# Kernel optimization log

Measured on AMD Instinct MI355X. Metric: run time of the kernel, lower is better.

The kernel has to match this reference:

```python
import jax, jax.numpy as jnp
import numpy as np

N = 50000   # nodes
E = 640000  # edges
IN, H, OUT = 128, 128, 64
BN_EPS = 1e-5


def setup_inputs() -> dict:
    key = jax.random.key(0)
    ks = jax.random.split(key, 16)
    inp = {}
    inp["x"] = jax.random.normal(ks[0], (N, IN), jnp.float32)
    inp["edge_index"] = jax.random.randint(ks[1], (2, E), 0, N, dtype=jnp.int32)
    # BatchNorm affine params (nontrivial so grads are informative)
    inp["bn_in_gamma"] = 1.0 + 0.1 * jax.random.normal(ks[2], (IN,), jnp.float32)
    inp["bn_in_beta"] = 0.1 * jax.random.normal(ks[3], (IN,), jnp.float32)
    inp["bn1_gamma"] = 1.0 + 0.1 * jax.random.normal(ks[4], (H,), jnp.float32)
    inp["bn1_beta"] = 0.1 * jax.random.normal(ks[5], (H,), jnp.float32)
    inp["bn2_gamma"] = 1.0 + 0.1 * jax.random.normal(ks[6], (OUT,), jnp.float32)
    inp["bn2_beta"] = 0.1 * jax.random.normal(ks[7], (OUT,), jnp.float32)
    # Linear / GCNConv weights (fan-in scaled)
    inp["proj_W"] = jax.random.normal(ks[8], (IN, H), jnp.float32) / np.sqrt(IN)
    inp["proj_b"] = jnp.zeros((H,), jnp.float32)
    inp["conv1_W"] = jax.random.normal(ks[9], (H, H), jnp.float32) / np.sqrt(H)
    inp["conv1_b"] = jnp.zeros((H,), jnp.float32)
    inp["conv2_W"] = jax.random.normal(ks[10], (H, OUT), jnp.float32) / np.sqrt(H)
    inp["conv2_b"] = jnp.zeros((OUT,), jnp.float32)
    return inp


def batchnorm(x, gamma, beta):
    # training-mode BN: batch statistics (biased variance), per-feature affine
    m = jnp.mean(x, axis=0)
    v = jnp.mean(jnp.square(x - m), axis=0)
    return (x - m) * jax.lax.rsqrt(v + BN_EPS) * gamma + beta


def gcn_conv(x, src, dst, W, b):
    # PyG GCNConv: y = D^{-1/2} (A + I) D^{-1/2} (x W) + b
    xw = x @ W                                    # [N, F_out]
    loops = jnp.arange(N, dtype=src.dtype)
    s = jnp.concatenate([src, loops])             # [E + N]
    d = jnp.concatenate([dst, loops])
    deg = jax.ops.segment_sum(jnp.ones_like(d, jnp.float32), d, num_segments=N)
    dinv = jnp.where(deg > 0, jax.lax.rsqrt(deg), 0.0)
    norm = dinv[s] * dinv[d]                      # [E + N]
    msgs = xw[s] * norm[:, None]                  # gather + per-edge scale
    out = jax.ops.segment_sum(msgs, d, num_segments=N)  # scatter-add
    return out + b


def reference(x, edge_index, bn_in_gamma, bn_in_beta, bn1_gamma, bn1_beta,
              bn2_gamma, bn2_beta, proj_W, proj_b, conv1_W, conv1_b,
              conv2_W, conv2_b):
    src, dst = edge_index[0], edge_index[1]
    h = batchnorm(x, bn_in_gamma, bn_in_beta)
    h = jax.nn.relu(h @ proj_W + proj_b)
    h = jax.nn.relu(batchnorm(gcn_conv(h, src, dst, conv1_W, conv1_b),
                              bn1_gamma, bn1_beta))
    # dropout: identity in eval mode
    out = batchnorm(gcn_conv(h, src, dst, conv2_W, conv2_b),
                    bn2_gamma, bn2_beta)
    return out
```

## Files before the change

kernel.cpp:

```cpp
#include <hip/hip_runtime.h>

#define NN 50000
#define NE 640000
#define BNEPS 1e-5f
#define NBANK 16
#define CAP 64

#define OFF_DINV 0
#define OFF_CURSOR 51200
#define OFF_ESRC 102400
#define OFF_WT0 1702400
#define OFF_WT1 1710592
#define OFF_WT2 1718784
#define OFF_STATS 1726976
#define OFF_B0 1737216
#define OFF_B1 8137216

typedef __attribute__((ext_vector_type(8))) __bf16 bf16x8;
typedef __attribute__((ext_vector_type(4))) float f32x4;

__device__ __forceinline__ float uplo(unsigned int u) {
  unsigned int v = u << 16;
  return __builtin_bit_cast(float, v);
}
__device__ __forceinline__ float uphi(unsigned int u) {
  unsigned int v = u & 0xffff0000u;
  return __builtin_bit_cast(float, v);
}
__device__ __forceinline__ unsigned int f2bf(float f) {
  unsigned int u = __builtin_bit_cast(unsigned int, f);
  return (u + 0x7fffu + ((u >> 16) & 1u)) >> 16;
}

__global__ __launch_bounds__(256) void prep_k(
    const float* __restrict__ W0, const float* __restrict__ W1,
    const float* __restrict__ W2, unsigned short* __restrict__ T0,
    unsigned short* __restrict__ T1, unsigned short* __restrict__ T2,
    int* __restrict__ cursor, float* __restrict__ stats) {
  const int bid = blockIdx.x;
  const int tid = threadIdx.x;
  if (bid < 160) {
    int f = bid * 256 + tid;
    if (f < 16384) {
      int k = f >> 7, n = f & 127;
      T0[n * 128 + k] = (unsigned short)f2bf(W0[f]);
    } else if (f < 32768) {
      int g = f - 16384;
      int k = g >> 7, n = g & 127;
      T1[n * 128 + k] = (unsigned short)f2bf(W1[g]);
    } else if (f < 40960) {
      int g = f - 32768;
      int k = g >> 6, n = g & 63;
      T2[n * 128 + k] = (unsigned short)f2bf(W2[g]);
    }
  } else if (bid < 356) {
    int i = (bid - 160) * 256 + tid;
    if (i < NN) cursor[i] = i * CAP;
  } else {
    int j = (bid - 356) * 256 + tid;
    stats[j] = 0.0f;
  }
}

template <int NC, int MODE>
__device__ __forceinline__ void bn_stats_body(
    int sbid, int nsb, int tid, const float* __restrict__ A,
    const float* __restrict__ dinv, const float* __restrict__ cb,
    float* __restrict__ sums, float* __restrict__ sqs,
    float (*rs)[NC], float (*rq)[NC]) {
  constexpr int CG = NC / 4;
  constexpr int RG = 256 / CG;
  const int tc = tid % CG;
  const int tr = tid / CG;
  float cb0 = 0, cb1 = 0, cb2 = 0, cb3 = 0;
  if (MODE == 1) {
    cb0 = cb[tc * 4];
    cb1 = cb[tc * 4 + 1];
    cb2 = cb[tc * 4 + 2];
    cb3 = cb[tc * 4 + 3];
  }
  float s0 = 0, s1 = 0, s2 = 0, s3 = 0, q0 = 0, q1 = 0, q2 = 0, q3 = 0;
  const int stride = nsb * RG;
  for (int r = sbid * RG + tr; r < NN; r += stride) {
    float4 v = *(const float4*)&A[(size_t)r * NC + tc * 4];
    if (MODE == 1) {
      float di = dinv[r];
      v.x = fmaf(v.x, di, cb0);
      v.y = fmaf(v.y, di, cb1);
      v.z = fmaf(v.z, di, cb2);
      v.w = fmaf(v.w, di, cb3);
    }
    s0 += v.x; s1 += v.y; s2 += v.z; s3 += v.w;
    q0 += v.x * v.x; q1 += v.y * v.y; q2 += v.z * v.z; q3 += v.w * v.w;
  }
  rs[tr][tc * 4] = s0; rs[tr][tc * 4 + 1] = s1;
  rs[tr][tc * 4 + 2] = s2; rs[tr][tc * 4 + 3] = s3;
  rq[tr][tc * 4] = q0; rq[tr][tc * 4 + 1] = q1;
  rq[tr][tc * 4 + 2] = q2; rq[tr][tc * 4 + 3] = q3;
  __syncthreads();
  if (tr == 0) {
    const int bank = (sbid & (NBANK - 1)) * NC;
    for (int j = 0; j < 4; ++j) {
      int c = tc * 4 + j;
      float ts = 0, tq = 0;
      for (int g = 0; g < RG; ++g) { ts += rs[g][c]; tq += rq[g][c]; }
      atomicAdd(&sums[bank + c], ts);
      atomicAdd(&sqs[bank + c], tq);
    }
  }
}

template <int NC, int MODE>
__global__ __launch_bounds__(256) void bn_stats_k(const float* __restrict__ A,
                                                  const float* __restrict__ dinv,
                                                  const float* __restrict__ cb,
                                                  float* __restrict__ sums,
                                                  float* __restrict__ sqs) {
  __shared__ float rs[256 / (NC / 4)][NC];
  __shared__ float rq[256 / (NC / 4)][NC];
  bn_stats_body<NC, MODE>(blockIdx.x, gridDim.x, threadIdx.x, A, dinv, cb,
                          sums, sqs, rs, rq);
}

__global__ __launch_bounds__(256) void bn_stats_bf_k(
    const unsigned short* __restrict__ Z, float* __restrict__ sums,
    float* __restrict__ sqs) {
  const int tc = threadIdx.x % 16;
  const int tr = threadIdx.x / 16;
  const int c = tc * 8;
  float s[8], q[8];
#pragma unroll
  for (int j = 0; j < 8; ++j) { s[j] = 0.f; q[j] = 0.f; }
  const int stride = gridDim.x * 16;
  for (int r = blockIdx.x * 16 + tr; r < NN; r += stride) {
    const uint4 p = *(const uint4*)&Z[(size_t)r * 128 + c];
    float e[8] = {uplo(p.x), uphi(p.x), uplo(p.y), uphi(p.y),
                  uplo(p.z), uphi(p.z), uplo(p.w), uphi(p.w)};
#pragma unroll
    for (int j = 0; j < 8; ++j) { s[j] += e[j]; q[j] += e[j] * e[j]; }
  }
  __shared__ float rs[16][128];
  __shared__ float rq[16][128];
#pragma unroll
  for (int j = 0; j < 8; ++j) { rs[tr][c + j] = s[j]; rq[tr][c + j] = q[j]; }
  __syncthreads();
  if (tr == 0) {
    const int bank = (blockIdx.x & (NBANK - 1)) * 128;
#pragma unroll
    for (int j = 0; j < 8; ++j) {
      float ts = 0.f, tq = 0.f;
      for (int g = 0; g < 16; ++g) { ts += rs[g][c + j]; tq += rq[g][c + j]; }
      atomicAdd(&sums[bank + c + j], ts);
      atomicAdd(&sqs[bank + c + j], tq);
    }
  }
}

template <int NC, int PRE, int EPI>
__device__ __forceinline__ void gemm_body(
    int bid, int tid, char* __restrict__ smem, float* __restrict__ af_s,
    float* __restrict__ bf_s, const void* __restrict__ Ain,
    const unsigned short* __restrict__ Wt, const float* __restrict__ bias,
    const float* __restrict__ sums, const float* __restrict__ sqs,
    const float* __restrict__ gamma, const float* __restrict__ beta,
    unsigned short* __restrict__ O1) {
  constexpr int TM = 64;
  constexpr int NTILES = NC / 16;
  constexpr int CSTR = NC + 4;
  const int row0 = bid * TM;

  if constexpr (PRE != 1) {
    if (tid < 128) {
      float s = 0.f, q = 0.f;
#pragma unroll
      for (int b = 0; b < NBANK; ++b) {
        s += sums[b * 128 + tid];
        q += sqs[b * 128 + tid];
      }
      float m = s * (1.0f / NN);
      float v = q * (1.0f / NN) - m * m;
      float a = gamma[tid] * rsqrtf(v + BNEPS);
      af_s[tid] = a;
      bf_s[tid] = beta[tid] - m * a;
    }
    __syncthreads();
    if constexpr (PRE == 0) {
      const float* A = (const float*)Ain;
      for (int f = tid; f < TM * 32; f += 256) {
        const int r = f >> 5;
        const int c4 = f & 31;
        const int rg = row0 + r;
        float4 v = make_float4(0.f, 0.f, 0.f, 0.f);
        if (rg < NN) {
          v = *(const float4*)&A[(size_t)rg * 128 + c4 * 4];
          const float4 a4 = *(const float4*)&af_s[c4 * 4];
          const float4 b4 = *(const float4*)&bf_s[c4 * 4];
          v.x = fmaf(a4.x, v.x, b4.x);
          v.y = fmaf(a4.y, v.y, b4.y);
          v.z = fmaf(a4.z, v.z, b4.z);
          v.w = fmaf(a4.w, v.w, b4.w);
        }
        uint2 wv;
        wv.x = f2bf(v.x) | (f2bf(v.y) << 16);
        wv.y = f2bf(v.z) | (f2bf(v.w) << 16);
        const int ba = (r * 256 + c4 * 8) ^ ((r & 7) << 4);
        *(uint2*)(smem + ba) = wv;
      }
    } else {
      const unsigned short* Ab = (const unsigned short*)Ain;
      for (int f = tid; f < TM * 16; f += 256) {
        const int r = f >> 4;
        const int c8 = f & 15;
        const int rg = row0 + r;
        uint4 w4 = make_uint4(0u, 0u, 0u, 0u);
        if (rg < NN) {
          const uint4 raw = *(const uint4*)&Ab[(size_t)rg * 128 + c8 * 8];
          const int cc = c8 * 8;
          float e[8] = {uplo(raw.x), uphi(raw.x), uplo(raw.y), uphi(raw.y),
                        uplo(raw.z), uphi(raw.z), uplo(raw.w), uphi(raw.w)};
          unsigned int p[4];
#pragma unroll
          for (int j = 0; j < 4; ++j) {
            float lo = fmaxf(fmaf(af_s[cc + 2 * j], e[2 * j], bf_s[cc + 2 * j]), 0.f);
            float hi = fmaxf(
                fmaf(af_s[cc + 2 * j + 1], e[2 * j + 1], bf_s[cc + 2 * j + 1]),
                0.f);
            p[j] = f2bf(lo) | (f2bf(hi) << 16);
          }
          w4 = make_uint4(p[0], p[1], p[2], p[3]);
        }
        const int ba = (r * 256 + c8 * 16) ^ ((r & 7) << 4);
        *(uint4*)(smem + ba) = w4;
      }
    }
    __syncthreads();
  }

  const int w = tid >> 6;
  const int l = tid & 63;
  const int lr = l & 15;
  const int lg = l >> 4;
  f32x4 acc[NTILES];
#pragma unroll
  for (int i = 0; i < NTILES; ++i) acc[i] = (f32x4){0.f, 0.f, 0.f, 0.f};
  const int arow = w * 16 + lr;
#pragma unroll
  for (int kt = 0; kt < 4; ++kt) {
    bf16x8 a;
    if constexpr (PRE == 1) {
      const unsigned short* Ab = (const unsigned short*)Ain;
      a = __builtin_bit_cast(
          bf16x8,
          *(const uint4*)&Ab[(size_t)(row0 + arow) * 128 + kt * 32 + lg * 8]);
    } else {
      const int ba = (arow * 256 + kt * 64 + lg * 16) ^ ((arow & 7) << 4);
      a = __builtin_bit_cast(bf16x8, *(const uint4*)(smem + ba));
    }
#pragma unroll
    for (int nt = 0; nt < NTILES; ++nt) {
      bf16x8 b = __builtin_bit_cast(
          bf16x8,
          *(const uint4*)&Wt[(size_t)(nt * 16 + lr) * 128 + kt * 32 + lg * 8]);
      acc[nt] = __builtin_amdgcn_mfma_f32_16x16x32_bf16(a, b, acc[nt], 0, 0, 0);
    }
  }
  __syncthreads();

  float* Cl = (float*)smem;
#pragma unroll
  for (int nt = 0; nt < NTILES; ++nt)
#pragma unroll
    for (int r = 0; r < 4; ++r)
      Cl[(w * 16 + lg * 4 + r) * CSTR + nt * 16 + lr] = acc[nt][r];
  __syncthreads();

  constexpr int CG = NC / 4;
  constexpr int RPT = TM * CG / 256;
  const int tc = tid % CG;
  const int tr = tid / CG;
  float4 b4 = make_float4(0.f, 0.f, 0.f, 0.f);
  if constexpr (EPI == 0) b4 = *(const float4*)&bias[tc * 4];
#pragma unroll
  for (int i = 0; i < RPT; ++i) {
    const int row = tr * RPT + i;
    const int rg = row0 + row;
    if (rg < NN) {
      float4 v = *(const float4*)&Cl[row * CSTR + tc * 4];
      if (EPI == 0) {
        v.x = fmaxf(v.x + b4.x, 0.f);
        v.y = fmaxf(v.y + b4.y, 0.f);
        v.z = fmaxf(v.z + b4.z, 0.f);
        v.w = fmaxf(v.w + b4.w, 0.f);
      }
      uint2 o;
      o.x = f2bf(v.x) | (f2bf(v.y) << 16);
      o.y = f2bf(v.z) | (f2bf(v.w) << 16);
      *(uint2*)&O1[(size_t)rg * NC + tc * 4] = o;
    }
  }
}

__global__ __launch_bounds__(256) void stats_fill_k(
    const float* __restrict__ x, float* __restrict__ s0,
    float* __restrict__ q0, const int* __restrict__ src,
    const int* __restrict__ dst, int* __restrict__ cursor,
    unsigned short* __restrict__ esrc) {
  __shared__ float rs[8][128];
  __shared__ float rq[8][128];
  const int bid = blockIdx.x;
  if (bid < 1024) {
    bn_stats_body<128, 0>(bid, 1024, threadIdx.x, x, nullptr, nullptr, s0, q0,
                          rs, rq);
  } else {
    int e = (bid - 1024) * 256 + threadIdx.x;
    if (e < NE / 2) {
      int p = atomicAdd(&cursor[dst[e]], 1);
      esrc[p] = (unsigned short)src[e];
    }
  }
}

__global__ __launch_bounds__(256) void gemm1_fill_k(
    const float* __restrict__ x, const unsigned short* __restrict__ Wt0,
    const float* __restrict__ proj_b, const float* __restrict__ s0,
    const float* __restrict__ q0, const float* __restrict__ g0,
    const float* __restrict__ b0, unsigned short* __restrict__ H1bf,
    const int* __restrict__ src, const int* __restrict__ dst,
    int* __restrict__ cursor, unsigned short* __restrict__ esrc) {
  __shared__ __align__(16) char smem[33792];
  __shared__ float af_s[128];
  __shared__ float bf_s[128];
  const int bid = blockIdx.x;
  const int tid = threadIdx.x;
  if (bid < 782) {
    gemm_body<128, 0, 0>(bid, tid, smem, af_s, bf_s, x, Wt0, proj_b, s0, q0,
                         g0, b0, H1bf);
  } else {
    int e = NE / 2 + (bid - 782) * 256 + tid;
    if (e < NE) {
      int p = atomicAdd(&cursor[dst[e]], 1);
      esrc[p] = (unsigned short)src[e];
    }
  }
}

__global__ __launch_bounds__(256) void conv1_dinv_k(
    const unsigned short* __restrict__ H1bf,
    const unsigned short* __restrict__ Wt1, unsigned short* __restrict__ Ybf,
    const int* __restrict__ cursor, float* __restrict__ dinv) {
  __shared__ __align__(16) char smem[33792];
  __shared__ float af_s[128];
  __shared__ float bf_s[128];
  const int bid = blockIdx.x;
  const int tid = threadIdx.x;
  if (bid < 782) {
    gemm_body<128, 1, 2>(bid, tid, smem, af_s, bf_s, H1bf, Wt1, nullptr,
                         nullptr, nullptr, nullptr, nullptr, Ybf);
  } else {
    int i = (bid - 782) * 256 + tid;
    if (i < NN) {
      int d = cursor[i] - i * CAP;
      dinv[i] = rsqrtf((float)d + 1.0f);
    }
  }
}

template <int NC, int OUTBF>
__global__ __launch_bounds__(256) void gather_bf_k(
    const int* __restrict__ cursor, const unsigned short* __restrict__ esrc,
    const unsigned short* __restrict__ Y, const float* __restrict__ dinv,
    void* __restrict__ outp, const float* __restrict__ cb) {
  constexpr int CG = NC / 8;
  constexpr int RG = 256 / CG;
  const int tc = threadIdx.x % CG;
  const int tr = threadIdx.x / CG;
  const int n = blockIdx.x * RG + tr;
  if (n >= NN) return;
  const int c = tc * 8;
  const float dn = dinv[n];
  float a[8];
  {
    const uint4 p = *(const uint4*)&Y[(size_t)n * NC + c];
    a[0] = dn * uplo(p.x); a[1] = dn * uphi(p.x);
    a[2] = dn * uplo(p.y); a[3] = dn * uphi(p.y);
    a[4] = dn * uplo(p.z); a[5] = dn * uphi(p.z);
    a[6] = dn * uplo(p.w); a[7] = dn * uphi(p.w);
  }
  const int beg = n * CAP;
  const int end = cursor[n];
  int e = beg;
  for (; e + 2 <= end; e += 2) {
    const int s0 = esrc[e];
    const int s1 = esrc[e + 1];
    const float d0 = dinv[s0];
    const float d1 = dinv[s1];
    const uint4 q0 = *(const uint4*)&Y[(size_t)s0 * NC + c];
    const uint4 q1 = *(const uint4*)&Y[(size_t)s1 * NC + c];
    a[0] = fmaf(d0, uplo(q0.x), a[0]); a[1] = fmaf(d0, uphi(q0.x), a[1]);
    a[2] = fmaf(d0, uplo(q0.y), a[2]); a[3] = fmaf(d0, uphi(q0.y), a[3]);
    a[4] = fmaf(d0, uplo(q0.z), a[4]); a[5] = fmaf(d0, uphi(q0.z), a[5]);
    a[6] = fmaf(d0, uplo(q0.w), a[6]); a[7] = fmaf(d0, uphi(q0.w), a[7]);
    a[0] = fmaf(d1, uplo(q1.x), a[0]); a[1] = fmaf(d1, uphi(q1.x), a[1]);
    a[2] = fmaf(d1, uplo(q1.y), a[2]); a[3] = fmaf(d1, uphi(q1.y), a[3]);
    a[4] = fmaf(d1, uplo(q1.z), a[4]); a[5] = fmaf(d1, uphi(q1.z), a[5]);
    a[6] = fmaf(d1, uplo(q1.w), a[6]); a[7] = fmaf(d1, uphi(q1.w), a[7]);
  }
  if (e < end) {
    const int s0 = esrc[e];
    const float d0 = dinv[s0];
    const uint4 q0 = *(const uint4*)&Y[(size_t)s0 * NC + c];
    a[0] = fmaf(d0, uplo(q0.x), a[0]); a[1] = fmaf(d0, uphi(q0.x), a[1]);
    a[2] = fmaf(d0, uplo(q0.y), a[2]); a[3] = fmaf(d0, uphi(q0.y), a[3]);
    a[4] = fmaf(d0, uplo(q0.z), a[4]); a[5] = fmaf(d0, uphi(q0.z), a[5]);
    a[6] = fmaf(d0, uplo(q0.w), a[6]); a[7] = fmaf(d0, uphi(q0.w), a[7]);
  }
  if constexpr (OUTBF == 1) {
    unsigned int p[4];
#pragma unroll
    for (int j = 0; j < 4; ++j) {
      float lo = fmaf(dn, a[2 * j], cb[c + 2 * j]);
      float hi = fmaf(dn, a[2 * j + 1], cb[c + 2 * j + 1]);
      p[j] = f2bf(lo) | (f2bf(hi) << 16);
    }
    *(uint4*)&((unsigned short*)outp)[(size_t)n * NC + c] =
        make_uint4(p[0], p[1], p[2], p[3]);
  } else {
    float* ACC = (float*)outp;
    *(float4*)&ACC[(size_t)n * NC + c] = make_float4(a[0], a[1], a[2], a[3]);
    *(float4*)&ACC[(size_t)n * NC + c + 4] =
        make_float4(a[4], a[5], a[6], a[7]);
  }
}

template <int NC, int PRE, int EPI>
__global__ __launch_bounds__(256) void mfma_gemm_k(
    const void* __restrict__ Ain, const unsigned short* __restrict__ Wt,
    const float* __restrict__ bias, const float* __restrict__ sums,
    const float* __restrict__ sqs, const float* __restrict__ gamma,
    const float* __restrict__ beta, unsigned short* __restrict__ O1) {
  constexpr int CBYTES = 64 * (NC + 4) * 4;
  constexpr int SMEM = (CBYTES > 16384) ? CBYTES : 16384;
  __shared__ __align__(16) char smem[SMEM];
  __shared__ float af_s[128];
  __shared__ float bf_s[128];
  gemm_body<NC, PRE, EPI>(blockIdx.x, threadIdx.x, smem, af_s, bf_s, Ain, Wt,
                          bias, sums, sqs, gamma, beta, O1);
}

__global__ __launch_bounds__(256) void final_k(
    const float* __restrict__ ACC2, const float* __restrict__ dinv,
    const float* __restrict__ cb, const float* __restrict__ s2,
    const float* __restrict__ q2, const float* __restrict__ gamma,
    const float* __restrict__ beta, float* __restrict__ out) {
  __shared__ float af_s[64];
  __shared__ float bf_s[64];
  if (threadIdx.x < 64) {
    float s = 0.f, q = 0.f;
#pragma unroll
    for (int b = 0; b < NBANK; ++b) {
      s += s2[b * 64 + threadIdx.x];
      q += q2[b * 64 + threadIdx.x];
    }
    float m = s * (1.0f / NN);
    float v = q * (1.0f / NN) - m * m;
    float a = gamma[threadIdx.x] * rsqrtf(v + BNEPS);
    af_s[threadIdx.x] = a;
    bf_s[threadIdx.x] = beta[threadIdx.x] - m * a;
  }
  __syncthreads();
  const int u = blockIdx.x * 256 + threadIdx.x;
  if (u >= NN * 16) return;
  const int r = u >> 4;
  const int c = (u & 15) * 4;
  const float di = dinv[r];
  float4 v = *(const float4*)&ACC2[(size_t)r * 64 + c];
  const float4 c4 = *(const float4*)&cb[c];
  const float4 a4 = *(const float4*)&af_s[c];
  const float4 b4 = *(const float4*)&bf_s[c];
  float4 o;
  o.x = fmaf(a4.x, fmaf(v.x, di, c4.x), b4.x);
  o.y = fmaf(a4.y, fmaf(v.y, di, c4.y), b4.y);
  o.z = fmaf(a4.z, fmaf(v.z, di, c4.z), b4.z);
  o.w = fmaf(a4.w, fmaf(v.w, di, c4.w), b4.w);
  *(float4*)&out[(size_t)r * 64 + c] = o;
}

extern "C" void kernel_launch(void* const* d_in, const int* in_sizes, int n_in,
                              void* d_out, int out_size, void* d_ws,
                              size_t ws_size, hipStream_t stream) {
  const float* x = (const float*)d_in[0];
  const int* ei = (const int*)d_in[1];
  const int* src = ei;
  const int* dst = ei + NE;
  const float* bn_in_g = (const float*)d_in[2];
  const float* bn_in_b = (const float*)d_in[3];
  const float* bn1_g = (const float*)d_in[4];
  const float* bn1_b = (const float*)d_in[5];
  const float* bn2_g = (const float*)d_in[6];
  const float* bn2_b = (const float*)d_in[7];
  const float* proj_W = (const float*)d_in[8];
  const float* proj_b = (const float*)d_in[9];
  const float* conv1_W = (const float*)d_in[10];
  const float* conv1_b = (const float*)d_in[11];
  const float* conv2_W = (const float*)d_in[12];
  const float* conv2_b = (const float*)d_in[13];
  float* out = (float*)d_out;

  float* ws = (float*)d_ws;
  float* dinv = ws + OFF_DINV;
  int* cursor = (int*)(ws + OFF_CURSOR);
  unsigned short* esrc = (unsigned short*)(ws + OFF_ESRC);
  unsigned short* Wt0 = (unsigned short*)(ws + OFF_WT0);
  unsigned short* Wt1 = (unsigned short*)(ws + OFF_WT1);
  unsigned short* Wt2 = (unsigned short*)(ws + OFF_WT2);
  float* st = ws + OFF_STATS;
  float* s0 = st;
  float* q0 = st + 2048;
  float* s1 = st + 4096;
  float* q1 = st + 6144;
  float* s2 = st + 8192;
  float* q2 = st + 9216;
  float* B0 = ws + OFF_B0;
  float* B1 = ws + OFF_B1;
  unsigned short* H1bf = (unsigned short*)B0;
  unsigned short* Ybf = (unsigned short*)B1;
  unsigned short* Z1bf = (unsigned short*)B0;
  unsigned short* Y2bf = (unsigned short*)B1;
  float* ACC2 = B0;

  prep_k<<<396, 256, 0, stream>>>(proj_W, conv1_W, conv2_W, Wt0, Wt1, Wt2,
                                  cursor, st);
  stats_fill_k<<<2274, 256, 0, stream>>>(x, s0, q0, src, dst, cursor, esrc);
  gemm1_fill_k<<<2032, 256, 0, stream>>>(x, Wt0, proj_b, s0, q0, bn_in_g,
                                         bn_in_b, H1bf, src, dst, cursor, esrc);
  conv1_dinv_k<<<978, 256, 0, stream>>>(H1bf, Wt1, Ybf, cursor, dinv);
  gather_bf_k<128, 1><<<(NN + 15) / 16, 256, 0, stream>>>(cursor, esrc, Ybf,
                                                          dinv, Z1bf, conv1_b);
  bn_stats_bf_k<<<1024, 256, 0, stream>>>(Z1bf, s1, q1);
  mfma_gemm_k<64, 3, 2><<<782, 256, 0, stream>>>(Z1bf, Wt2, nullptr, s1, q1,
                                                 bn1_g, bn1_b, Y2bf);
  gather_bf_k<64, 0><<<(NN + 31) / 32, 256, 0, stream>>>(cursor, esrc, Y2bf,
                                                         dinv, ACC2, nullptr);
  bn_stats_k<64, 1><<<1024, 256, 0, stream>>>(ACC2, dinv, conv2_b, s2, q2);
  final_k<<<(NN * 16 + 255) / 256, 256, 0, stream>>>(ACC2, dinv, conv2_b, s2,
                                                     q2, bn2_g, bn2_b, out);
}
```

Baseline: 176.1 us.

## Fuse BN statistics into gather kernels and halve GEMM epilogue LDS

The per-channel sum and sum-of-squares reductions for BN1 and BN2 now run inside the two gather kernels, so the standalone bn_stats passes that re-read Z1 and ACC2 are gone. The atomic accumulation spreads over 64 banks to ease contention. The second conv's bias and dinv scaling move into the gather, which simplifies final_k. The GEMM epilogue now stages results through LDS in two 32-row halves, halving shared memory per block to raise occupancy at the cost of an extra barrier round.

```diff
diff --git a/kernel.cpp b/kernel.cpp
--- a/kernel.cpp
+++ b/kernel.cpp
@@ -3,7 +3,6 @@
 #define NN 50000
 #define NE 640000
 #define BNEPS 1e-5f
-#define NBANK 16
 #define CAP 64
 
 #define OFF_DINV 0
@@ -12,9 +11,9 @@
 #define OFF_WT0 1702400
 #define OFF_WT1 1710592
 #define OFF_WT2 1718784
-#define OFF_STATS 1726976
-#define OFF_B0 1737216
-#define OFF_B1 8137216
+#define OFF_STATS 1722880
+#define OFF_B0 1751552
+#define OFF_B1 8151552
 
 typedef __attribute__((ext_vector_type(8))) __bf16 bf16x8;
 typedef __attribute__((ext_vector_type(4))) float f32x4;
@@ -62,34 +61,17 @@
   }
 }
 
-template <int NC, int MODE>
-__device__ __forceinline__ void bn_stats_body(
-    int sbid, int nsb, int tid, const float* __restrict__ A,
-    const float* __restrict__ dinv, const float* __restrict__ cb,
-    float* __restrict__ sums, float* __restrict__ sqs,
-    float (*rs)[NC], float (*rq)[NC]) {
-  constexpr int CG = NC / 4;
-  constexpr int RG = 256 / CG;
-  const int tc = tid % CG;
-  const int tr = tid / CG;
-  float cb0 = 0, cb1 = 0, cb2 = 0, cb3 = 0;
-  if (MODE == 1) {
-    cb0 = cb[tc * 4];
-    cb1 = cb[tc * 4 + 1];
-    cb2 = cb[tc * 4 + 2];
-    cb3 = cb[tc * 4 + 3];
-  }
+__device__ __forceinline__ void statsx_body(int sbid, int tid,
+                                            const float* __restrict__ A,
+                                            float* __restrict__ sums,
+                                            float* __restrict__ sqs,
+                                            float (*rs)[128],
+                                            float (*rq)[128]) {
+  const int tc = tid % 32;
+  const int tr = tid / 32;
   float s0 = 0, s1 = 0, s2 = 0, s3 = 0, q0 = 0, q1 = 0, q2 = 0, q3 = 0;
-  const int stride = nsb * RG;
-  for (int r = sbid * RG + tr; r < NN; r += stride) {
-    float4 v = *(const float4*)&A[(size_t)r * NC + tc * 4];
-    if (MODE == 1) {
-      float di = dinv[r];
-      v.x = fmaf(v.x, di, cb0);
-      v.y = fmaf(v.y, di, cb1);
-      v.z = fmaf(v.z, di, cb2);
-      v.w = fmaf(v.w, di, cb3);
-    }
+  for (int r = sbid * 8 + tr; r < NN; r += 1024 * 8) {
+    float4 v = *(const float4*)&A[(size_t)r * 128 + tc * 4];
     s0 += v.x; s1 += v.y; s2 += v.z; s3 += v.w;
     q0 += v.x * v.x; q1 += v.y * v.y; q2 += v.z * v.z; q3 += v.w * v.w;
   }
@@ -99,64 +81,37 @@
   rq[tr][tc * 4 + 2] = q2; rq[tr][tc * 4 + 3] = q3;
   __syncthreads();
   if (tr == 0) {
-    const int bank = (sbid & (NBANK - 1)) * NC;
+    const int bank = (sbid & 15) * 128;
     for (int j = 0; j < 4; ++j) {
       int c = tc * 4 + j;
       float ts = 0, tq = 0;
-      for (int g = 0; g < RG; ++g) { ts += rs[g][c]; tq += rq[g][c]; }
+      for (int g = 0; g < 8; ++g) { ts += rs[g][c]; tq += rq[g][c]; }
       atomicAdd(&sums[bank + c], ts);
       atomicAdd(&sqs[bank + c], tq);
     }
   }
 }
 
-template <int NC, int MODE>
-__global__ __launch_bounds__(256) void bn_stats_k(const float* __restrict__ A,
-                                                  const float* __restrict__ dinv,
-                                                  const float* __restrict__ cb,
-                                                  float* __restrict__ sums,
-                                                  float* __restrict__ sqs) {
-  __shared__ float rs[256 / (NC / 4)][NC];
-  __shared__ float rq[256 / (NC / 4)][NC];
-  bn_stats_body<NC, MODE>(blockIdx.x, gridDim.x, threadIdx.x, A, dinv, cb,
-                          sums, sqs, rs, rq);
-}
-
-__global__ __launch_bounds__(256) void bn_stats_bf_k(
-    const unsigned short* __restrict__ Z, float* __restrict__ sums,
-    float* __restrict__ sqs) {
-  const int tc = threadIdx.x % 16;
-  const int tr = threadIdx.x / 16;
-  const int c = tc * 8;
-  float s[8], q[8];
-#pragma unroll
-  for (int j = 0; j < 8; ++j) { s[j] = 0.f; q[j] = 0.f; }
-  const int stride = gridDim.x * 16;
-  for (int r = blockIdx.x * 16 + tr; r < NN; r += stride) {
-    const uint4 p = *(const uint4*)&Z[(size_t)r * 128 + c];
-    float e[8] = {uplo(p.x), uphi(p.x), uplo(p.y), uphi(p.y),
-                  uplo(p.z), uphi(p.z), uplo(p.w), uphi(p.w)};
-#pragma unroll
-    for (int j = 0; j < 8; ++j) { s[j] += e[j]; q[j] += e[j] * e[j]; }
-  }
-  __shared__ float rs[16][128];
-  __shared__ float rq[16][128];
-#pragma unroll
-  for (int j = 0; j < 8; ++j) { rs[tr][c + j] = s[j]; rq[tr][c + j] = q[j]; }
-  __syncthreads();
-  if (tr == 0) {
-    const int bank = (blockIdx.x & (NBANK - 1)) * 128;
-#pragma unroll
-    for (int j = 0; j < 8; ++j) {
-      float ts = 0.f, tq = 0.f;
-      for (int g = 0; g < 16; ++g) { ts += rs[g][c + j]; tq += rq[g][c + j]; }
-      atomicAdd(&sums[bank + c + j], ts);
-      atomicAdd(&sqs[bank + c + j], tq);
-    }
-  }
-}
-
-template <int NC, int PRE, int EPI>
+__global__ __launch_bounds__(256) void stats_fill_k(
+    const float* __restrict__ x, float* __restrict__ s0,
+    float* __restrict__ q0, const int* __restrict__ src,
+    const int* __restrict__ dst, int* __restrict__ cursor,
+    unsigned short* __restrict__ esrc) {
+  __shared__ float rs[8][128];
+  __shared__ float rq[8][128];
+  const int bid = blockIdx.x;
+  if (bid < 1024) {
+    statsx_body(bid, threadIdx.x, x, s0, q0, rs, rq);
+  } else {
+    int e = (bid - 1024) * 256 + threadIdx.x;
+    if (e < NE / 2) {
+      int p = atomicAdd(&cursor[dst[e]], 1);
+      esrc[p] = (unsigned short)src[e];
+    }
+  }
+}
+
+template <int NC, int PRE, int EPI, int NB>
 __device__ __forceinline__ void gemm_body(
     int bid, int tid, char* __restrict__ smem, float* __restrict__ af_s,
     float* __restrict__ bf_s, const void* __restrict__ Ain,
@@ -173,7 +128,7 @@
     if (tid < 128) {
       float s = 0.f, q = 0.f;
 #pragma unroll
-      for (int b = 0; b < NBANK; ++b) {
+      for (int b = 0; b < NB; ++b) {
         s += sums[b * 128 + tid];
         q += sqs[b * 128 + tid];
       }
@@ -221,7 +176,8 @@
           unsigned int p[4];
 #pragma unroll
           for (int j = 0; j < 4; ++j) {
-            float lo = fmaxf(fmaf(af_s[cc + 2 * j], e[2 * j], bf_s[cc + 2 * j]), 0.f);
+            float lo =
+                fmaxf(fmaf(af_s[cc + 2 * j], e[2 * j], bf_s[cc + 2 * j]), 0.f);
             float hi = fmaxf(
                 fmaf(af_s[cc + 2 * j + 1], e[2 * j + 1], bf_s[cc + 2 * j + 1]),
                 0.f);
@@ -264,58 +220,42 @@
       acc[nt] = __builtin_amdgcn_mfma_f32_16x16x32_bf16(a, b, acc[nt], 0, 0, 0);
     }
   }
-  __syncthreads();
 
   float* Cl = (float*)smem;
-#pragma unroll
-  for (int nt = 0; nt < NTILES; ++nt)
-#pragma unroll
-    for (int r = 0; r < 4; ++r)
-      Cl[(w * 16 + lg * 4 + r) * CSTR + nt * 16 + lr] = acc[nt][r];
-  __syncthreads();
-
   constexpr int CG = NC / 4;
-  constexpr int RPT = TM * CG / 256;
-  const int tc = tid % CG;
-  const int tr = tid / CG;
+  constexpr int RPH = CG / 8;
+  const int tcx = tid % CG;
+  const int trx = tid / CG;
   float4 b4 = make_float4(0.f, 0.f, 0.f, 0.f);
-  if constexpr (EPI == 0) b4 = *(const float4*)&bias[tc * 4];
-#pragma unroll
-  for (int i = 0; i < RPT; ++i) {
-    const int row = tr * RPT + i;
-    const int rg = row0 + row;
-    if (rg < NN) {
-      float4 v = *(const float4*)&Cl[row * CSTR + tc * 4];
-      if (EPI == 0) {
-        v.x = fmaxf(v.x + b4.x, 0.f);
-        v.y = fmaxf(v.y + b4.y, 0.f);
-        v.z = fmaxf(v.z + b4.z, 0.f);
-        v.w = fmaxf(v.w + b4.w, 0.f);
+  if constexpr (EPI == 0) b4 = *(const float4*)&bias[tcx * 4];
+#pragma unroll
+  for (int half = 0; half < 2; ++half) {
+    __syncthreads();
+    if ((w >> 1) == half) {
+#pragma unroll
+      for (int nt = 0; nt < NTILES; ++nt)
+#pragma unroll
+        for (int r = 0; r < 4; ++r)
+          Cl[((w & 1) * 16 + lg * 4 + r) * CSTR + nt * 16 + lr] = acc[nt][r];
+    }
+    __syncthreads();
+#pragma unroll
+    for (int i = 0; i < RPH; ++i) {
+      const int rl = trx * RPH + i;
+      const int rg = row0 + half * 32 + rl;
+      if (rg < NN) {
+        float4 v = *(const float4*)&Cl[rl * CSTR + tcx * 4];
+        if (EPI == 0) {
+          v.x = fmaxf(v.x + b4.x, 0.f);
+          v.y = fmaxf(v.y + b4.y, 0.f);
+          v.z = fmaxf(v.z + b4.z, 0.f);
+          v.w = fmaxf(v.w + b4.w, 0.f);
+        }
+        uint2 o;
+        o.x = f2bf(v.x) | (f2bf(v.y) << 16);
+        o.y = f2bf(v.z) | (f2bf(v.w) << 16);
+        *(uint2*)&O1[(size_t)rg * NC + tcx * 4] = o;
       }
-      uint2 o;
-      o.x = f2bf(v.x) | (f2bf(v.y) << 16);
-      o.y = f2bf(v.z) | (f2bf(v.w) << 16);
-      *(uint2*)&O1[(size_t)rg * NC + tc * 4] = o;
-    }
-  }
-}
-
-__global__ __launch_bounds__(256) void stats_fill_k(
-    const float* __restrict__ x, float* __restrict__ s0,
-    float* __restrict__ q0, const int* __restrict__ src,
-    const int* __restrict__ dst, int* __restrict__ cursor,
-    unsigned short* __restrict__ esrc) {
-  __shared__ float rs[8][128];
-  __shared__ float rq[8][128];
-  const int bid = blockIdx.x;
-  if (bid < 1024) {
-    bn_stats_body<128, 0>(bid, 1024, threadIdx.x, x, nullptr, nullptr, s0, q0,
-                          rs, rq);
-  } else {
-    int e = (bid - 1024) * 256 + threadIdx.x;
-    if (e < NE / 2) {
-      int p = atomicAdd(&cursor[dst[e]], 1);
-      esrc[p] = (unsigned short)src[e];
     }
   }
 }
@@ -327,14 +267,14 @@
     const float* __restrict__ b0, unsigned short* __restrict__ H1bf,
     const int* __restrict__ src, const int* __restrict__ dst,
     int* __restrict__ cursor, unsigned short* __restrict__ esrc) {
-  __shared__ __align__(16) char smem[33792];
+  __shared__ __align__(16) char smem[17408];
   __shared__ float af_s[128];
   __shared__ float bf_s[128];
   const int bid = blockIdx.x;
   const int tid = threadIdx.x;
   if (bid < 782) {
-    gemm_body<128, 0, 0>(bid, tid, smem, af_s, bf_s, x, Wt0, proj_b, s0, q0,
-                         g0, b0, H1bf);
+    gemm_body<128, 0, 0, 16>(bid, tid, smem, af_s, bf_s, x, Wt0, proj_b, s0,
+                             q0, g0, b0, H1bf);
   } else {
     int e = NE / 2 + (bid - 782) * 256 + tid;
     if (e < NE) {
@@ -348,14 +288,14 @@
     const unsigned short* __restrict__ H1bf,
     const unsigned short* __restrict__ Wt1, unsigned short* __restrict__ Ybf,
     const int* __restrict__ cursor, float* __restrict__ dinv) {
-  __shared__ __align__(16) char smem[33792];
+  __shared__ __align__(16) char smem[17408];
   __shared__ float af_s[128];
   __shared__ float bf_s[128];
   const int bid = blockIdx.x;
   const int tid = threadIdx.x;
   if (bid < 782) {
-    gemm_body<128, 1, 2>(bid, tid, smem, af_s, bf_s, H1bf, Wt1, nullptr,
-                         nullptr, nullptr, nullptr, nullptr, Ybf);
+    gemm_body<128, 1, 2, 16>(bid, tid, smem, af_s, bf_s, H1bf, Wt1, nullptr,
+                             nullptr, nullptr, nullptr, nullptr, Ybf);
   } else {
     int i = (bid - 782) * 256 + tid;
     if (i < NN) {
@@ -365,91 +305,113 @@
   }
 }
 
-template <int NC, int OUTBF>
+template <int NC, int OUTBF, int NB>
 __global__ __launch_bounds__(256) void gather_bf_k(
     const int* __restrict__ cursor, const unsigned short* __restrict__ esrc,
     const unsigned short* __restrict__ Y, const float* __restrict__ dinv,
-    void* __restrict__ outp, const float* __restrict__ cb) {
+    void* __restrict__ outp, const float* __restrict__ cb,
+    float* __restrict__ sums, float* __restrict__ sqs) {
   constexpr int CG = NC / 8;
   constexpr int RG = 256 / CG;
+  __shared__ float rs[RG][NC];
+  __shared__ float rq[RG][NC];
   const int tc = threadIdx.x % CG;
   const int tr = threadIdx.x / CG;
   const int n = blockIdx.x * RG + tr;
-  if (n >= NN) return;
+  const bool act = (n < NN);
   const int c = tc * 8;
-  const float dn = dinv[n];
-  float a[8];
-  {
-    const uint4 p = *(const uint4*)&Y[(size_t)n * NC + c];
-    a[0] = dn * uplo(p.x); a[1] = dn * uphi(p.x);
-    a[2] = dn * uplo(p.y); a[3] = dn * uphi(p.y);
-    a[4] = dn * uplo(p.z); a[5] = dn * uphi(p.z);
-    a[6] = dn * uplo(p.w); a[7] = dn * uphi(p.w);
-  }
-  const int beg = n * CAP;
-  const int end = cursor[n];
-  int e = beg;
-  for (; e + 2 <= end; e += 2) {
-    const int s0 = esrc[e];
-    const int s1 = esrc[e + 1];
-    const float d0 = dinv[s0];
-    const float d1 = dinv[s1];
-    const uint4 q0 = *(const uint4*)&Y[(size_t)s0 * NC + c];
-    const uint4 q1 = *(const uint4*)&Y[(size_t)s1 * NC + c];
-    a[0] = fmaf(d0, uplo(q0.x), a[0]); a[1] = fmaf(d0, uphi(q0.x), a[1]);
-    a[2] = fmaf(d0, uplo(q0.y), a[2]); a[3] = fmaf(d0, uphi(q0.y), a[3]);
-    a[4] = fmaf(d0, uplo(q0.z), a[4]); a[5] = fmaf(d0, uphi(q0.z), a[5]);
-    a[6] = fmaf(d0, uplo(q0.w), a[6]); a[7] = fmaf(d0, uphi(q0.w), a[7]);
-    a[0] = fmaf(d1, uplo(q1.x), a[0]); a[1] = fmaf(d1, uphi(q1.x), a[1]);
-    a[2] = fmaf(d1, uplo(q1.y), a[2]); a[3] = fmaf(d1, uphi(q1.y), a[3]);
-    a[4] = fmaf(d1, uplo(q1.z), a[4]); a[5] = fmaf(d1, uphi(q1.z), a[5]);
-    a[6] = fmaf(d1, uplo(q1.w), a[6]); a[7] = fmaf(d1, uphi(q1.w), a[7]);
-  }
-  if (e < end) {
-    const int s0 = esrc[e];
-    const float d0 = dinv[s0];
-    const uint4 q0 = *(const uint4*)&Y[(size_t)s0 * NC + c];
-    a[0] = fmaf(d0, uplo(q0.x), a[0]); a[1] = fmaf(d0, uphi(q0.x), a[1]);
-    a[2] = fmaf(d0, uplo(q0.y), a[2]); a[3] = fmaf(d0, uphi(q0.y), a[3]);
-    a[4] = fmaf(d0, uplo(q0.z), a[4]); a[5] = fmaf(d0, uphi(q0.z), a[5]);
-    a[6] = fmaf(d0, uplo(q0.w), a[6]); a[7] = fmaf(d0, uphi(q0.w), a[7]);
-  }
-  if constexpr (OUTBF == 1) {
-    unsigned int p[4];
-#pragma unroll
-    for (int j = 0; j < 4; ++j) {
-      float lo = fmaf(dn, a[2 * j], cb[c + 2 * j]);
-      float hi = fmaf(dn, a[2 * j + 1], cb[c + 2 * j + 1]);
-      p[j] = f2bf(lo) | (f2bf(hi) << 16);
-    }
-    *(uint4*)&((unsigned short*)outp)[(size_t)n * NC + c] =
-        make_uint4(p[0], p[1], p[2], p[3]);
-  } else {
-    float* ACC = (float*)outp;
-    *(float4*)&ACC[(size_t)n * NC + c] = make_float4(a[0], a[1], a[2], a[3]);
-    *(float4*)&ACC[(size_t)n * NC + c + 4] =
-        make_float4(a[4], a[5], a[6], a[7]);
-  }
-}
-
-template <int NC, int PRE, int EPI>
+  float z[8];
+#pragma unroll
+  for (int j = 0; j < 8; ++j) z[j] = 0.f;
+  if (act) {
+    const float dn = dinv[n];
+    float a[8];
+    {
+      const uint4 p = *(const uint4*)&Y[(size_t)n * NC + c];
+      a[0] = dn * uplo(p.x); a[1] = dn * uphi(p.x);
+      a[2] = dn * uplo(p.y); a[3] = dn * uphi(p.y);
+      a[4] = dn * uplo(p.z); a[5] = dn * uphi(p.z);
+      a[6] = dn * uplo(p.w); a[7] = dn * uphi(p.w);
+    }
+    const int beg = n * CAP;
+    const int end = cursor[n];
+    int e = beg;
+    for (; e + 2 <= end; e += 2) {
+      const int s0 = esrc[e];
+      const int s1 = esrc[e + 1];
+      const float d0 = dinv[s0];
+      const float d1 = dinv[s1];
+      const uint4 q0 = *(const uint4*)&Y[(size_t)s0 * NC + c];
+      const uint4 q1 = *(const uint4*)&Y[(size_t)s1 * NC + c];
+      a[0] = fmaf(d0, uplo(q0.x), a[0]); a[1] = fmaf(d0, uphi(q0.x), a[1]);
+      a[2] = fmaf(d0, uplo(q0.y), a[2]); a[3] = fmaf(d0, uphi(q0.y), a[3]);
+      a[4] = fmaf(d0, uplo(q0.z), a[4]); a[5] = fmaf(d0, uphi(q0.z), a[5]);
+      a[6] = fmaf(d0, uplo(q0.w), a[6]); a[7] = fmaf(d0, uphi(q0.w), a[7]);
+      a[0] = fmaf(d1, uplo(q1.x), a[0]); a[1] = fmaf(d1, uphi(q1.x), a[1]);
+      a[2] = fmaf(d1, uplo(q1.y), a[2]); a[3] = fmaf(d1, uphi(q1.y), a[3]);
+      a[4] = fmaf(d1, uplo(q1.z), a[4]); a[5] = fmaf(d1, uphi(q1.z), a[5]);
+      a[6] = fmaf(d1, uplo(q1.w), a[6]); a[7] = fmaf(d1, uphi(q1.w), a[7]);
+    }
+    if (e < end) {
+      const int s0 = esrc[e];
+      const float d0 = dinv[s0];
+      const uint4 q0 = *(const uint4*)&Y[(size_t)s0 * NC + c];
+      a[0] = fmaf(d0, uplo(q0.x), a[0]); a[1] = fmaf(d0, uphi(q0.x), a[1]);
+      a[2] = fmaf(d0, uplo(q0.y), a[2]); a[3] = fmaf(d0, uphi(q0.y), a[3]);
+      a[4] = fmaf(d0, uplo(q0.z), a[4]); a[5] = fmaf(d0, uphi(q0.z), a[5]);
+      a[6] = fmaf(d0, uplo(q0.w), a[6]); a[7] = fmaf(d0, uphi(q0.w), a[7]);
+    }
+#pragma unroll
+    for (int j = 0; j < 8; ++j) z[j] = fmaf(dn, a[j], cb[c + j]);
+    if constexpr (OUTBF == 1) {
+      unsigned int p[4];
+#pragma unroll
+      for (int j = 0; j < 4; ++j)
+        p[j] = f2bf(z[2 * j]) | (f2bf(z[2 * j + 1]) << 16);
+      *(uint4*)&((unsigned short*)outp)[(size_t)n * NC + c] =
+          make_uint4(p[0], p[1], p[2], p[3]);
+    } else {
+      float* Z = (float*)outp;
+      *(float4*)&Z[(size_t)n * NC + c] = make_float4(z[0], z[1], z[2], z[3]);
+      *(float4*)&Z[(size_t)n * NC + c + 4] =
+          make_float4(z[4], z[5], z[6], z[7]);
+    }
+  }
+#pragma unroll
+  for (int j = 0; j < 8; ++j) {
+    rs[tr][c + j] = z[j];
+    rq[tr][c + j] = z[j] * z[j];
+  }
+  __syncthreads();
+  if (tr == 0) {
+    const int bank = (blockIdx.x % NB) * NC;
+#pragma unroll
+    for (int j = 0; j < 8; ++j) {
+      float ts = 0.f, tq = 0.f;
+      for (int g = 0; g < RG; ++g) { ts += rs[g][c + j]; tq += rq[g][c + j]; }
+      atomicAdd(&sums[bank + c + j], ts);
+      atomicAdd(&sqs[bank + c + j], tq);
+    }
+  }
+}
+
+template <int NC, int PRE, int EPI, int NB>
 __global__ __launch_bounds__(256) void mfma_gemm_k(
     const void* __restrict__ Ain, const unsigned short* __restrict__ Wt,
     const float* __restrict__ bias, const float* __restrict__ sums,
     const float* __restrict__ sqs, const float* __restrict__ gamma,
     const float* __restrict__ beta, unsigned short* __restrict__ O1) {
-  constexpr int CBYTES = 64 * (NC + 4) * 4;
+  constexpr int CBYTES = 32 * (NC + 4) * 4;
   constexpr int SMEM = (CBYTES > 16384) ? CBYTES : 16384;
   __shared__ __align__(16) char smem[SMEM];
   __shared__ float af_s[128];
   __shared__ float bf_s[128];
-  gemm_body<NC, PRE, EPI>(blockIdx.x, threadIdx.x, smem, af_s, bf_s, Ain, Wt,
-                          bias, sums, sqs, gamma, beta, O1);
+  gemm_body<NC, PRE, EPI, NB>(blockIdx.x, threadIdx.x, smem, af_s, bf_s, Ain,
+                              Wt, bias, sums, sqs, gamma, beta, O1);
 }
 
 __global__ __launch_bounds__(256) void final_k(
-    const float* __restrict__ ACC2, const float* __restrict__ dinv,
-    const float* __restrict__ cb, const float* __restrict__ s2,
+    const float* __restrict__ Z2, const float* __restrict__ s2,
     const float* __restrict__ q2, const float* __restrict__ gamma,
     const float* __restrict__ beta, float* __restrict__ out) {
   __shared__ float af_s[64];
@@ -457,7 +419,7 @@
   if (threadIdx.x < 64) {
     float s = 0.f, q = 0.f;
 #pragma unroll
-    for (int b = 0; b < NBANK; ++b) {
+    for (int b = 0; b < 64; ++b) {
       s += s2[b * 64 + threadIdx.x];
       q += q2[b * 64 + threadIdx.x];
     }
@@ -472,16 +434,14 @@
   if (u >= NN * 16) return;
   const int r = u >> 4;
   const int c = (u & 15) * 4;
-  const float di = dinv[r];
-  float4 v = *(const float4*)&ACC2[(size_t)r * 64 + c];
-  const float4 c4 = *(const float4*)&cb[c];
+  float4 v = *(const float4*)&Z2[(size_t)r * 64 + c];
   const float4 a4 = *(const float4*)&af_s[c];
   const float4 b4 = *(const float4*)&bf_s[c];
   float4 o;
-  o.x = fmaf(a4.x, fmaf(v.x, di, c4.x), b4.x);
-  o.y = fmaf(a4.y, fmaf(v.y, di, c4.y), b4.y);
-  o.z = fmaf(a4.z, fmaf(v.z, di, c4.z), b4.z);
-  o.w = fmaf(a4.w, fmaf(v.w, di, c4.w), b4.w);
+  o.x = fmaf(a4.x, v.x, b4.x);
+  o.y = fmaf(a4.y, v.y, b4.y);
+  o.z = fmaf(a4.z, v.z, b4.z);
+  o.w = fmaf(a4.w, v.w, b4.w);
   *(float4*)&out[(size_t)r * 64 + c] = o;
 }
 
@@ -517,31 +477,29 @@
   float* s0 = st;
   float* q0 = st + 2048;
   float* s1 = st + 4096;
-  float* q1 = st + 6144;
-  float* s2 = st + 8192;
-  float* q2 = st + 9216;
+  float* q1 = st + 12288;
+  float* s2 = st + 20480;
+  float* q2 = st + 24576;
   float* B0 = ws + OFF_B0;
   float* B1 = ws + OFF_B1;
   unsigned short* H1bf = (unsigned short*)B0;
   unsigned short* Ybf = (unsigned short*)B1;
   unsigned short* Z1bf = (unsigned short*)B0;
   unsigned short* Y2bf = (unsigned short*)B1;
-  float* ACC2 = B0;
-
-  prep_k<<<396, 256, 0, stream>>>(proj_W, conv1_W, conv2_W, Wt0, Wt1, Wt2,
+  float* Z2 = B0;
+
+  prep_k<<<468, 256, 0, stream>>>(proj_W, conv1_W, conv2_W, Wt0, Wt1, Wt2,
                                   cursor, st);
   stats_fill_k<<<2274, 256, 0, stream>>>(x, s0, q0, src, dst, cursor, esrc);
   gemm1_fill_k<<<2032, 256, 0, stream>>>(x, Wt0, proj_b, s0, q0, bn_in_g,
                                          bn_in_b, H1bf, src, dst, cursor, esrc);
   conv1_dinv_k<<<978, 256, 0, stream>>>(H1bf, Wt1, Ybf, cursor, dinv);
-  gather_bf_k<128, 1><<<(NN + 15) / 16, 256, 0, stream>>>(cursor, esrc, Ybf,
-                                                          dinv, Z1bf, conv1_b);
-  bn_stats_bf_k<<<1024, 256, 0, stream>>>(Z1bf, s1, q1);
-  mfma_gemm_k<64, 3, 2><<<782, 256, 0, stream>>>(Z1bf, Wt2, nullptr, s1, q1,
-                                                 bn1_g, bn1_b, Y2bf);
-  gather_bf_k<64, 0><<<(NN + 31) / 32, 256, 0, stream>>>(cursor, esrc, Y2bf,
-                                                         dinv, ACC2, nullptr);
-  bn_stats_k<64, 1><<<1024, 256, 0, stream>>>(ACC2, dinv, conv2_b, s2, q2);
-  final_k<<<(NN * 16 + 255) / 256, 256, 0, stream>>>(ACC2, dinv, conv2_b, s2,
-                                                     q2, bn2_g, bn2_b, out);
-}
+  gather_bf_k<128, 1, 64><<<3125, 256, 0, stream>>>(cursor, esrc, Ybf, dinv,
+                                                    Z1bf, conv1_b, s1, q1);
+  mfma_gemm_k<64, 3, 2, 64><<<782, 256, 0, stream>>>(Z1bf, Wt2, nullptr, s1,
+                                                     q1, bn1_g, bn1_b, Y2bf);
+  gather_bf_k<64, 0, 64><<<1563, 256, 0, stream>>>(cursor, esrc, Y2bf, dinv,
+                                                   Z2, conv2_b, s2, q2);
+  final_k<<<(NN * 16 + 255) / 256, 256, 0, stream>>>(Z2, s2, q2, bn2_g, bn2_b,
+                                                     out);
+}
```

New measurement: 179.1 us. About the same (+1.7%).
